# Performance work log

Measured on AMD Instinct MI355X. Metric: run time of the kernel, lower is better.

Reference implementation:

```python
import jax, jax.numpy as jnp
import numpy as np

HID = 128
HEADS = 8
HDIM = HID // HEADS
MLP = int(HID * 4.0)
N = 50000
E = 800000
EPS = 1e-6


def _ln(x):
    m = jnp.mean(x, axis=-1, keepdims=True)
    v = jnp.var(x, axis=-1, keepdims=True)
    return (x - m) / jnp.sqrt(v + EPS)


def _modulate(x, shift, scale):
    return x * (1 + scale) + shift


def setup_inputs() -> dict:
    key = jax.random.key(0)
    ks = jax.random.split(key, 12)
    s = lambda fan_in: 1.0 / np.sqrt(fan_in)
    return {
        "x": jax.random.normal(ks[0], (N, HID), dtype=jnp.float32),
        "edge_index": jax.random.randint(ks[1], (2, E), 0, N, dtype=jnp.int64),
        "c": jax.random.normal(ks[2], (N, HID), dtype=jnp.float32),
        "w_qkv": jax.random.normal(ks[3], (HID, 3 * HID), dtype=jnp.float32) * s(HID),
        "w_proj": jax.random.normal(ks[4], (HID, HID), dtype=jnp.float32) * s(HID),
        "b_proj": jnp.zeros((HID,), dtype=jnp.float32),
        "w_mlp1": jax.random.normal(ks[5], (HID, MLP), dtype=jnp.float32) * s(HID),
        "b_mlp1": jnp.zeros((MLP,), dtype=jnp.float32),
        "w_mlp2": jax.random.normal(ks[6], (MLP, HID), dtype=jnp.float32) * s(MLP),
        "b_mlp2": jnp.zeros((HID,), dtype=jnp.float32),
        "w_ada": jax.random.normal(ks[7], (HID, 6 * HID), dtype=jnp.float32) * s(HID),
        "b_ada": jnp.zeros((6 * HID,), dtype=jnp.float32),
    }


def _graph_attn(x, edge_index, w_qkv, w_proj, b_proj):
    n = x.shape[0]
    qkv = x @ w_qkv  # [N, 3*HID]
    q, k, v = jnp.split(qkv, 3, axis=-1)
    q = q.reshape(n, HEADS, HDIM)
    k = k.reshape(n, HEADS, HDIM)
    v = v.reshape(n, HEADS, HDIM)
    src = edge_index[0]  # j (source)
    dst = edge_index[1]  # i (destination / aggregation key)
    # per-edge attention score [E, HEADS]
    score = jnp.einsum('ehd,ehd->eh', q[dst], k[src]) / np.sqrt(HDIM)
    # segment softmax over destination node
    smax = jax.ops.segment_max(score, dst, num_segments=n)  # [N, H]
    ex = jnp.exp(score - smax[dst])
    den = jax.ops.segment_sum(ex, dst, num_segments=n)
    attn = ex / den[dst]  # [E, H]
    msg = v[src] * attn[:, :, None]  # [E, H, D]
    out = jax.ops.segment_sum(msg, dst, num_segments=n)  # [N, H, D]
    return out.reshape(n, HID) @ w_proj + b_proj


def reference(x, edge_index, c, w_qkv, w_proj, b_proj, w_mlp1, b_mlp1,
              w_mlp2, b_mlp2, w_ada, b_ada):
    mods = jax.nn.silu(c) @ w_ada + b_ada
    sh_msa, sc_msa, g_msa, sh_mlp, sc_mlp, g_mlp = jnp.split(mods, 6, axis=-1)
    x = x + g_msa * _graph_attn(_modulate(_ln(x), sh_msa, sc_msa),
                                edge_index, w_qkv, w_proj, b_proj)
    h = _modulate(_ln(x), sh_mlp, sc_mlp)
    h = jax.nn.gelu(h @ w_mlp1 + b_mlp1, approximate=True) @ w_mlp2 + b_mlp2
    return x + g_mlp * h
```

## Files before the change

kernel.cpp:

```cpp
#include <hip/hip_runtime.h>
#include <math.h>

#define N_NODES 50000
#define HIDD 128
#define HEADS 8
#define HDIM 16
#define NE 800000

using short8 = __attribute__((ext_vector_type(8))) short;
using f32x4 = __attribute__((ext_vector_type(4))) float;

__device__ __forceinline__ int load_idx(const void* ei, int is64, long long pos) {
  long long v = is64 ? ((const long long*)ei)[pos]
                     : (long long)((const int*)ei)[pos];
  unsigned uv = (unsigned)v;
  return (uv < N_NODES) ? (int)uv : 0;
}

__global__ void detect_kernel(const unsigned* __restrict__ ei_raw, int* flag) {
  __shared__ int any_nonzero;
  if (threadIdx.x == 0) any_nonzero = 0;
  __syncthreads();
  if (threadIdx.x < 128) {
    if (ei_raw[2 * threadIdx.x + 1] != 0u) atomicOr(&any_nonzero, 1);
  }
  __syncthreads();
  if (threadIdx.x == 0) *flag = any_nonzero ? 0 : 1;
}

__global__ __launch_bounds__(256) void probe_kernel(float* out, int n, float mb) {
  int i = blockIdx.x * 256 + threadIdx.x;
  if (i < n) out[i] = (i == 0) ? mb : 0.f;
}

struct ProNone {
  __device__ __forceinline__ float operator()(float v, int, int) const { return v; }
};
struct EpiNone {
  __device__ __forceinline__ float operator()(float a, int, int) const { return a; }
};
struct EpiBias {
  const float* b;
  __device__ __forceinline__ float operator()(float a, int, int c) const { return a + b[c]; }
};
struct EpiGelu {
  const float* b;
  __device__ __forceinline__ float operator()(float a, int, int c) const {
    float t = a + b[c];
    float u = 0.7978845608028654f * (t + 0.044715f * t * t * t);
    float au = fabsf(u);
    float e = __expf(2.f * au);
    float th = __builtin_copysignf(1.f - 2.f / (e + 1.f), u);
    return 0.5f * t * (1.f + th);
  }
};
struct EpiResGateB {
  const float* b;
  const float* xres;
  const unsigned short* gate;
  __device__ __forceinline__ float operator()(float a, int r, int c) const {
    float g = __uint_as_float((unsigned)gate[(size_t)r * 768 + c] << 16);
    return xres[(size_t)r * HIDD + c] + g * (a + b[c]);
  }
};

struct CvTab {
  int end[8];
  int src_sel[8];
  int src_off[8];
  int ldb[8];
  int n[8];
  int dst_off[8];
};
__global__ __launch_bounds__(256) void convert_all_kernel(
    const float* __restrict__ p0, const float* __restrict__ p1,
    const float* __restrict__ p2, const float* __restrict__ p3,
    const float* __restrict__ p4, CvTab t, int total,
    unsigned short* __restrict__ hi) {
  int idx = blockIdx.x * 256 + threadIdx.x;
  if (idx >= total) return;
  int s = 0;
#pragma unroll
  for (int j = 0; j < 7; j++) s += (idx >= t.end[j]) ? 1 : 0;
  int local = idx - (s ? t.end[s - 1] : 0);
  int N = t.n[s];
  int k = (unsigned)local / (unsigned)N;
  int n = local - k * N;
  const float* B;
  int sel = t.src_sel[s];
  B = (sel == 0) ? p0 : (sel == 1) ? p1 : (sel == 2) ? p2 : (sel == 3) ? p3 : p4;
  float f = B[(size_t)k * t.ldb[s] + t.src_off[s] + n];
  unsigned u = __float_as_uint(f);
  unsigned short hs = (unsigned short)((u + 0x7FFFu + ((u >> 16) & 1u)) >> 16);
  int lane = (((k >> 3) & 3) << 4) | (n & 15);
  int dst = t.dst_off[s] + (((k >> 5) * (N >> 4) + (n >> 4)) * 64 + lane) * 8 + (k & 7);
  hi[dst] = hs;
}

__device__ __forceinline__ void split8(const float f[8], short8& ahi, short8& alo) {
  union { unsigned u[4]; short8 v; } ch, cl;
#pragma unroll
  for (int e = 0; e < 4; e++) {
    unsigned u0 = __float_as_uint(f[2 * e]);
    unsigned u1 = __float_as_uint(f[2 * e + 1]);
    ch.u[e] = (u0 >> 16) | (u1 & 0xFFFF0000u);
    float h0 = __uint_as_float(u0 & 0xFFFF0000u);
    float h1 = __uint_as_float(u1 & 0xFFFF0000u);
    cl.u[e] = (__float_as_uint(f[2 * e] - h0) >> 16) |
              (__float_as_uint(f[2 * e + 1] - h1) & 0xFFFF0000u);
  }
  ahi = ch.v;
  alo = cl.v;
}

template <class Pro, int AMODE>
__device__ __forceinline__ void load_a_frag(
    const void* __restrict__ Av, const void* __restrict__ Av2, int arow, int K,
    int kb, int quad, bool aok, Pro pro, short8& ahi, short8& alo) {
  ahi = {};
  alo = {};
  if constexpr (AMODE == 0) {
    const float* A = (const float*)Av;
    float4 a0 = make_float4(0.f, 0.f, 0.f, 0.f), a1 = a0;
    if (aok) {
      const float* ap = A + (size_t)arow * K + kb * 32 + quad * 8;
      a0 = *(const float4*)ap;
      a1 = *(const float4*)(ap + 4);
      int cb = kb * 32 + quad * 8;
      a0.x = pro(a0.x, arow, cb + 0); a0.y = pro(a0.y, arow, cb + 1);
      a0.z = pro(a0.z, arow, cb + 2); a0.w = pro(a0.w, arow, cb + 3);
      a1.x = pro(a1.x, arow, cb + 4); a1.y = pro(a1.y, arow, cb + 5);
      a1.z = pro(a1.z, arow, cb + 6); a1.w = pro(a1.w, arow, cb + 7);
    }
    float f[8] = {a0.x, a0.y, a0.z, a0.w, a1.x, a1.y, a1.z, a1.w};
    split8(f, ahi, alo);
  } else if constexpr (AMODE == 1) {
    if (aok)
      ahi = *(const short8*)((const unsigned short*)Av + (size_t)arow * K + kb * 32 + quad * 8);
  } else {
    if (aok) {
      size_t aoff = (size_t)arow * K + kb * 32 + quad * 8;
      ahi = *(const short8*)((const unsigned short*)Av + aoff);
      alo = *(const short8*)((const unsigned short*)Av2 + aoff);
    }
  }
}

template <class Epi, int OMODE, int NTC>
__device__ __forceinline__ void store_tiles(
    const f32x4* acc, void* __restrict__ Cv, int M, int N, int mrow0, int col0,
    int quad, int ln15, Epi epi) {
  float* C = (float*)Cv;
#pragma unroll
  for (int nt = 0; nt < NTC; nt++) {
    f32x4 a = acc[nt];
    int gc = col0 + nt * 16 + ln15;
#pragma unroll
    for (int r = 0; r < 4; r++) {
      int gr = mrow0 + quad * 4 + r;
      if (gr < M) {
        if constexpr (OMODE == 1) {
          float* crow = C + (size_t)gr * 256;
          if (gc < 128) {
            crow[gc] = a[r];
          } else {
            unsigned u = __float_as_uint(a[r]);
            unsigned rr = (u + 0x7FFFu + ((u >> 16) & 1u)) >> 16;
            unsigned short* kv = (unsigned short*)crow + 256;
            int c = gc - 128;
            int idx = (c < 128) ? (((c >> 2) << 3) + (c & 3))
                                : ((((c - 128) >> 2) << 3) + 4 + ((c - 128) & 3));
            kv[idx] = (unsigned short)rr;
          }
        } else if constexpr (OMODE == 2) {
          float v = epi(a[r], gr, gc);
          unsigned u = __float_as_uint(v);
          unsigned rr = (u + 0x7FFFu + ((u >> 16) & 1u)) >> 16;
          ((unsigned short*)Cv)[(size_t)gr * N + gc] = (unsigned short)rr;
        } else {
          C[(size_t)gr * N + gc] = epi(a[r], gr, gc);
        }
      }
    }
  }
}

template <class Pro, class Epi, int OMODE, int AMODE, int NTC, int KK, bool LDSB = false>
__global__ __launch_bounds__(256) void gemm_direct(
    const void* __restrict__ Av, const void* __restrict__ Av2,
    const unsigned short* __restrict__ B,
    void* __restrict__ Cv, int M, int N, Pro pro, Epi epi) {
  const int tid = threadIdx.x;
  const int lane = tid & 63;
  const int wv = tid >> 6;
  const int quad = lane >> 4;
  const int ln15 = lane & 15;
  const int mrow0 = blockIdx.x * 64 + wv * 16;
  const int arow = mrow0 + ln15;
  const int Nt = N >> 4;
  const bool aok = (arow < M);
  const int col0 = blockIdx.y * (NTC * 16);
  const int ntbase = col0 >> 4;
  constexpr int KB = KK >> 5;
  static_assert(!LDSB || KB == 4, "LDSB path assumes K==128 (4 kb, one per wave)");

  __shared__ short8 lbs[LDSB ? 4 * NTC * 64 : 1];
  if constexpr (LDSB) {
    const unsigned short* gb = B + ((size_t)(wv * Nt + ntbase) * 64 + lane) * 8;
#pragma unroll
    for (int nt = 0; nt < NTC; nt++)
      lbs[(wv * NTC + nt) * 64 + lane] = *(const short8*)(gb + nt * 512);
    __syncthreads();
  }

  f32x4 acc[NTC] = {};
#pragma unroll
  for (int kb = 0; kb < KB; kb++) {
    short8 ahi, alo;
    load_a_frag<Pro, AMODE>(Av, Av2, arow, KK, kb, quad, aok, pro, ahi, alo);
    const unsigned short* bp = B + ((size_t)(kb * Nt + ntbase) * 64 + lane) * 8;
#pragma unroll
    for (int nt = 0; nt < NTC; nt++) {
      short8 b;
      if constexpr (LDSB)
        b = lbs[(kb * NTC + nt) * 64 + lane];
      else
        b = *(const short8*)(bp + nt * 512);
      if constexpr (AMODE != 1)
        acc[nt] = __builtin_amdgcn_mfma_f32_16x16x32_bf16(alo, b, acc[nt], 0, 0, 0);
      acc[nt] = __builtin_amdgcn_mfma_f32_16x16x32_bf16(ahi, b, acc[nt], 0, 0, 0);
    }
  }
  store_tiles<Epi, OMODE, NTC>(acc, Cv, M, N, mrow0, col0, quad, ln15, epi);
}

__global__ __launch_bounds__(256) void silu_split_kernel(
    const float* __restrict__ c, unsigned* __restrict__ ch, unsigned* __restrict__ cl) {
  int wave = threadIdx.x >> 6;
  int lane = threadIdx.x & 63;
  int row = blockIdx.x * 4 + wave;
  if (row >= N_NODES) return;
  float2 v = *(const float2*)(c + (size_t)row * HIDD + lane * 2);
  float ox = v.x / (1.f + __expf(-v.x));
  float oy = v.y / (1.f + __expf(-v.y));
  unsigned ux = __float_as_uint(ox), uy = __float_as_uint(oy);
  unsigned hx = ux & 0xFFFF0000u, hy = uy & 0xFFFF0000u;
  unsigned lx = __float_as_uint(ox - __uint_as_float(hx));
  unsigned ly = __float_as_uint(oy - __uint_as_float(hy));
  ch[(size_t)row * 64 + lane] = (ux >> 16) | hy;
  cl[(size_t)row * 64 + lane] = (lx >> 16) | (ly & 0xFFFF0000u);
}

__global__ __launch_bounds__(256) void ln_mod_kernel(
    const float* __restrict__ x, const unsigned* __restrict__ sa,
    unsigned* __restrict__ xh, unsigned* __restrict__ xl) {
  int wave = threadIdx.x >> 6;
  int lane = threadIdx.x & 63;
  int row = blockIdx.x * 4 + wave;
  if (row >= N_NODES) return;
  float2 v = *(const float2*)(x + (size_t)row * HIDD + lane * 2);
  float s = v.x + v.y;
  float sq = v.x * v.x + v.y * v.y;
#pragma unroll
  for (int o = 32; o >= 1; o >>= 1) {
    s += __shfl_xor(s, o);
    sq += __shfl_xor(sq, o);
  }
  float m = s * (1.f / 128.f);
  float var = sq * (1.f / 128.f) - m * m;
  float rs = rsqrtf(var + 1e-6f);
  unsigned shw = sa[(size_t)row * 384 + lane];
  unsigned scw = sa[(size_t)row * 384 + 64 + lane];
  float shx = __uint_as_float(shw << 16), shy = __uint_as_float(shw & 0xFFFF0000u);
  float scx = __uint_as_float(scw << 16), scy = __uint_as_float(scw & 0xFFFF0000u);
  float ox = (v.x - m) * rs * (1.f + scx) + shx;
  float oy = (v.y - m) * rs * (1.f + scy) + shy;
  unsigned ux = __float_as_uint(ox), uy = __float_as_uint(oy);
  unsigned hx = ux & 0xFFFF0000u, hy = uy & 0xFFFF0000u;
  unsigned lx = __float_as_uint(ox - __uint_as_float(hx));
  unsigned ly = __float_as_uint(oy - __uint_as_float(hy));
  xh[(size_t)row * 64 + lane] = (ux >> 16) | hy;
  xl[(size_t)row * 64 + lane] = (lx >> 16) | (ly & 0xFFFF0000u);
}

__global__ __launch_bounds__(256) void zero_int_kernel(int* p, int n) {
  int i = blockIdx.x * 256 + threadIdx.x;
  if (i < n) p[i] = 0;
}

__global__ __launch_bounds__(256) void hist_kernel(const void* __restrict__ ei,
                                                   const int* __restrict__ flag,
                                                   int* __restrict__ A) {
  int e = blockIdx.x * 256 + threadIdx.x;
  if (e >= NE) return;
  int dst = load_idx(ei, *flag, (long long)NE + e);
  atomicAdd(&A[dst + 1], 1);
}

__global__ __launch_bounds__(1024) void scan1_kernel(int* __restrict__ A, int n,
                                                     int* __restrict__ bsum) {
  __shared__ int buf[2][1024];
  int i = blockIdx.x * 1024 + threadIdx.x;
  int val = (i < n) ? A[i] : 0;
  int pb = 0;
  buf[0][threadIdx.x] = val;
  __syncthreads();
#pragma unroll
  for (int off = 1; off < 1024; off <<= 1) {
    int t = buf[pb][threadIdx.x];
    if ((int)threadIdx.x >= off) t += buf[pb][threadIdx.x - off];
    buf[pb ^ 1][threadIdx.x] = t;
    pb ^= 1;
    __syncthreads();
  }
  int incl = buf[pb][threadIdx.x];
  if (i < n) A[i] = incl;
  if (threadIdx.x == 1023) bsum[blockIdx.x] = incl;
}
__global__ void scan2_kernel(int* __restrict__ bsum, int nb) {
  int l = threadIdx.x;
  int v = (l < nb) ? bsum[l] : 0;
#pragma unroll
  for (int off = 1; off < 64; off <<= 1) {
    int t = __shfl_up(v, off);
    if (l >= off) v += t;
  }
  if (l < nb) bsum[l] = v;
}
__global__ __launch_bounds__(256) void scan3_kernel(int* __restrict__ A, int n,
                                                    const int* __restrict__ bsum) {
  int i = blockIdx.x * 256 + threadIdx.x;
  int b = i >> 10;
  if (i < n && b > 0) A[i] += bsum[b - 1];
}

__global__ __launch_bounds__(256) void scatter_kernel(const void* __restrict__ ei,
                                                      const int* __restrict__ flag,
                                                      int* __restrict__ A,
                                                      unsigned short* __restrict__ col) {
  int e = blockIdx.x * 256 + threadIdx.x;
  if (e >= NE) return;
  int is64 = *flag;
  int src = load_idx(ei, is64, e);
  int dst = load_idx(ei, is64, (long long)NE + e);
  int pos = atomicAdd(&A[dst], 1);
  col[pos] = (unsigned short)src;
}

__global__ __launch_bounds__(256) void node_attn_kernel(
    const int* __restrict__ A, const unsigned short* __restrict__ col,
    const float* __restrict__ qkv, float* __restrict__ attn) {
  int wave = threadIdx.x >> 6;
  int lane = threadIdx.x & 63;
  int half = lane >> 5;
  int l32 = lane & 31;
  int node = blockIdx.x * 4 + wave;
  if (node >= N_NODES) return;
  int start = (node == 0) ? 0 : A[node - 1];
  int end = A[node];
  int deg = end - start;

  float4 q = *(const float4*)(qkv + (size_t)node * 256 + l32 * 4);
  float l = 0.f;
  float4 acc = make_float4(0.f, 0.f, 0.f, 0.f);

  if (deg > 0) {
    int itc = (deg + 1) >> 1;
    int last = end - 1;
    const unsigned* qu = (const unsigned*)qkv;
    auto eidx = [&](int it) {
      int e = start + 2 * it + half;
      return (e <= last) ? e : last;
    };
    int i2 = col[eidx(2)];
    uint4 kv0 = *(const uint4*)(qu + (size_t)col[eidx(0)] * 256 + 128 + 4 * l32);
    uint4 kv1 = *(const uint4*)(qu + (size_t)col[eidx(1)] * 256 + 128 + 4 * l32);
    for (int it = 0; it < itc; it++) {
      uint4 kv2 = *(const uint4*)(qu + (size_t)i2 * 256 + 128 + 4 * l32);
      i2 = col[eidx(it + 3)];
      float kx = __uint_as_float(kv0.x << 16);
      float ky = __uint_as_float(kv0.x & 0xFFFF0000u);
      float kz = __uint_as_float(kv0.y << 16);
      float kw = __uint_as_float(kv0.y & 0xFFFF0000u);
      float s = q.x * kx + q.y * ky + q.z * kz + q.w * kw;
      s += __shfl_xor(s, 1);
      s += __shfl_xor(s, 2);
      s *= 0.25f;
      bool valid = (start + 2 * it + half) < end;
      float w = valid ? __expf(fminf(s, 60.f)) : 0.f;
      float vx = __uint_as_float(kv0.z << 16);
      float vy = __uint_as_float(kv0.z & 0xFFFF0000u);
      float vz = __uint_as_float(kv0.w << 16);
      float vw = __uint_as_float(kv0.w & 0xFFFF0000u);
      l += w;
      acc.x += w * vx;
      acc.y += w * vy;
      acc.z += w * vz;
      acc.w += w * vw;
      kv0 = kv1;
      kv1 = kv2;
    }
  }
  l += __shfl_xor(l, 32);
  acc.x += __shfl_xor(acc.x, 32);
  acc.y += __shfl_xor(acc.y, 32);
  acc.z += __shfl_xor(acc.z, 32);
  acc.w += __shfl_xor(acc.w, 32);
  float inv = (l > 0.f) ? 1.f / l : 0.f;
  if (half == 0) {
    float4 o = make_float4(acc.x * inv, acc.y * inv, acc.z * inv, acc.w * inv);
    *(float4*)(attn + (size_t)node * HIDD + l32 * 4) = o;
  }
}

extern "C" void kernel_launch(void* const* d_in, const int* in_sizes, int n_in,
                              void* d_out, int out_size, void* d_ws, size_t ws_size,
                              hipStream_t stream) {
  const float* x      = (const float*)d_in[0];
  const void*  ei     = d_in[1];
  const float* c      = (const float*)d_in[2];
  const float* w_qkv  = (const float*)d_in[3];
  const float* w_proj = (const float*)d_in[4];
  const float* b_proj = (const float*)d_in[5];
  const float* w_mlp1 = (const float*)d_in[6];
  const float* b_mlp1 = (const float*)d_in[7];
  const float* w_mlp2 = (const float*)d_in[8];
  const float* b_mlp2 = (const float*)d_in[9];
  const float* w_ada  = (const float*)d_in[10];
  const float* b_ada  = (const float*)d_in[11];
  float* out = (float*)d_out;

  const size_t NM = (size_t)N_NODES;
  unsigned short* ada = (unsigned short*)d_ws;
  float* buf1 = (float*)(ada + NM * 768);
  float* buf2 = buf1 + NM * 128;
  int*   Arow  = (int*)(buf2 + NM * 256);
  unsigned short* col = (unsigned short*)(Arow + 50048);
  int*   eflag = (int*)(col + NE);
  int*   bsum  = eflag + 8;
  unsigned short* Bpl = (unsigned short*)(bsum + 64);
  unsigned* xh = (unsigned*)buf1;
  unsigned* xl = xh + NM * 64;
  float* attnb = buf1;
  unsigned* sch = (unsigned*)buf2;
  unsigned* scl = sch + NM * 64;
  float* qkv   = buf2;
  unsigned short* h1 = (unsigned short*)buf2;

  const int o_qkv = 0, o_ada = 49152, o_proj = 147456, o_mlp1 = 163840,
            o_mlp2 = 229376;
  const int cv_total = 294912;

  const size_t req_bytes = (NM * 768) * 4 + 50048 * 4 + NE * 2 + 32 + 256 +
                           (size_t)cv_total * 2;
  dim3 blk(256);
  if (ws_size < req_bytes) {
    probe_kernel<<<dim3((out_size + 255) / 256), blk, 0, stream>>>(
        out, out_size, (float)(ws_size >> 20));
    return;
  }

  const int MB = (N_NODES + 63) / 64;
  const int EB = (NE + 255) / 256;
  const int SB = (N_NODES + 1 + 1023) / 1024;

  detect_kernel<<<dim3(1), blk, 0, stream>>>((const unsigned*)ei, eflag);
  zero_int_kernel<<<dim3((N_NODES + 1 + 255) / 256), blk, 0, stream>>>(Arow, N_NODES + 1);
  hist_kernel<<<dim3(EB), blk, 0, stream>>>(ei, eflag, Arow);
  scan1_kernel<<<dim3(SB), dim3(1024), 0, stream>>>(Arow, N_NODES + 1, bsum);
  scan2_kernel<<<dim3(1), dim3(64), 0, stream>>>(bsum, SB);
  scan3_kernel<<<dim3((N_NODES + 1 + 255) / 256), blk, 0, stream>>>(Arow, N_NODES + 1, bsum);
  scatter_kernel<<<dim3(EB), blk, 0, stream>>>(ei, eflag, Arow, col);

  {
    CvTab t;
    int sel[8]     = { 0,      1,      2,      3,      4,      0, 0, 0 };
    int soff[8]    = { 0,      0,      0,      0,      0,      0, 0, 0 };
    int ldb[8]     = { 384,    768,    128,    512,    128,    1, 1, 1 };
    int nn[8]      = { 384,    768,    128,    512,    128,    1, 1, 1 };
    int doff[8]    = { o_qkv,  o_ada,  o_proj, o_mlp1, o_mlp2, 0, 0, 0 };
    int cnt[8]     = { 49152,  98304,  16384,  65536,  65536,  0, 0, 0 };
    int accum = 0;
    for (int s = 0; s < 8; s++) {
      accum += cnt[s];
      t.end[s] = accum; t.src_sel[s] = sel[s]; t.src_off[s] = soff[s];
      t.ldb[s] = ldb[s]; t.n[s] = nn[s]; t.dst_off[s] = doff[s];
    }
    convert_all_kernel<<<dim3((cv_total + 255) / 256), blk, 0, stream>>>(
        w_qkv, w_ada, w_proj, w_mlp1, w_mlp2, t, cv_total, Bpl);
  }

  silu_split_kernel<<<dim3((N_NODES + 3) / 4), blk, 0, stream>>>(c, sch, scl);

  gemm_direct<ProNone, EpiBias, 2, 2, 8, 128, true><<<dim3(MB, 6), blk, 0, stream>>>(
      sch, scl, Bpl + o_ada, ada, N_NODES, 768, ProNone{}, EpiBias{b_ada});

  ln_mod_kernel<<<dim3((N_NODES + 3) / 4), blk, 0, stream>>>(
      x, (const unsigned*)ada, xh, xl);

  gemm_direct<ProNone, EpiNone, 1, 2, 8, 128, true><<<dim3(MB, 3), blk, 0, stream>>>(
      xh, xl, Bpl + o_qkv, qkv, N_NODES, 384, ProNone{}, EpiNone{});

  node_attn_kernel<<<dim3((N_NODES + 3) / 4), blk, 0, stream>>>(Arow, col, qkv, attnb);

  gemm_direct<ProNone, EpiResGateB, 0, 0, 4, 128, true><<<dim3(MB, 2), blk, 0, stream>>>(
      attnb, nullptr, Bpl + o_proj, out, N_NODES, 128,
      ProNone{}, EpiResGateB{b_proj, x, ada + 256});

  ln_mod_kernel<<<dim3((N_NODES + 3) / 4), blk, 0, stream>>>(
      out, (const unsigned*)(ada + 384), xh, xl);

  gemm_direct<ProNone, EpiGelu, 2, 2, 8, 128, true><<<dim3(MB, 4), blk, 0, stream>>>(
      xh, xl, Bpl + o_mlp1, h1, N_NODES, 512, ProNone{}, EpiGelu{b_mlp1});

  gemm_direct<ProNone, EpiResGateB, 0, 1, 4, 512, false><<<dim3(MB, 2), blk, 0, stream>>>(
      h1, nullptr, Bpl + o_mlp2, out, N_NODES, 128,
      ProNone{}, EpiResGateB{b_mlp2, out, ada + 640});
}
```

Measured before the change: 502.1 us.

## Process four edges per wave with 8-wide K/V interleave in node attention

Changes the bf16 K/V interleave written by the QKV GEMM epilogue from groups of 4 to groups of 8 elements. The node attention kernel now has each 16-lane quarter handle one edge, so a wave processes four edges per iteration instead of two. Each lane loads 8 K and 8 V values, which removes one shuffle from the score reduction. The aim is more edges in flight per wave and fewer loop iterations on the gather-bound aggregation, at the cost of more registers and more final cross-lane reductions.

```diff
diff --git a/kernel.cpp b/kernel.cpp
--- a/kernel.cpp
+++ b/kernel.cpp
@@ -9,6 +9,9 @@
 
 using short8 = __attribute__((ext_vector_type(8))) short;
 using f32x4 = __attribute__((ext_vector_type(4))) float;
+
+__device__ __forceinline__ float bf_lo(unsigned u) { return __uint_as_float(u << 16); }
+__device__ __forceinline__ float bf_hi(unsigned u) { return __uint_as_float(u & 0xFFFF0000u); }
 
 __device__ __forceinline__ int load_idx(const void* ei, int is64, long long pos) {
   long long v = is64 ? ((const long long*)ei)[pos]
@@ -168,8 +171,8 @@
             unsigned rr = (u + 0x7FFFu + ((u >> 16) & 1u)) >> 16;
             unsigned short* kv = (unsigned short*)crow + 256;
             int c = gc - 128;
-            int idx = (c < 128) ? (((c >> 2) << 3) + (c & 3))
-                                : ((((c - 128) >> 2) << 3) + 4 + ((c - 128) & 3));
+            int idx = (c < 128) ? (((c >> 3) << 4) + (c & 7))
+                                : ((((c - 128) >> 3) << 4) + 8 + ((c - 128) & 7));
             kv[idx] = (unsigned short)rr;
           }
         } else if constexpr (OMODE == 2) {
@@ -352,64 +355,73 @@
     const float* __restrict__ qkv, float* __restrict__ attn) {
   int wave = threadIdx.x >> 6;
   int lane = threadIdx.x & 63;
-  int half = lane >> 5;
-  int l32 = lane & 31;
+  int qtr = lane >> 4;
+  int l16 = lane & 15;
   int node = blockIdx.x * 4 + wave;
   if (node >= N_NODES) return;
   int start = (node == 0) ? 0 : A[node - 1];
   int end = A[node];
   int deg = end - start;
 
-  float4 q = *(const float4*)(qkv + (size_t)node * 256 + l32 * 4);
+  const float* qp = qkv + (size_t)node * 256 + l16 * 8;
+  float4 q0 = *(const float4*)qp;
+  float4 q1 = *(const float4*)(qp + 4);
   float l = 0.f;
-  float4 acc = make_float4(0.f, 0.f, 0.f, 0.f);
+  float4 a0 = make_float4(0.f, 0.f, 0.f, 0.f);
+  float4 a1 = make_float4(0.f, 0.f, 0.f, 0.f);
 
   if (deg > 0) {
-    int itc = (deg + 1) >> 1;
+    int itc = (deg + 3) >> 2;
     int last = end - 1;
     const unsigned* qu = (const unsigned*)qkv;
     auto eidx = [&](int it) {
-      int e = start + 2 * it + half;
+      int e = start + 4 * it + qtr;
       return (e <= last) ? e : last;
     };
     int i2 = col[eidx(2)];
-    uint4 kv0 = *(const uint4*)(qu + (size_t)col[eidx(0)] * 256 + 128 + 4 * l32);
-    uint4 kv1 = *(const uint4*)(qu + (size_t)col[eidx(1)] * 256 + 128 + 4 * l32);
+    const unsigned* b0 = qu + (size_t)col[eidx(0)] * 256 + 128 + 8 * l16;
+    uint4 k0 = *(const uint4*)b0;
+    uint4 v0 = *(const uint4*)(b0 + 4);
+    const unsigned* b1 = qu + (size_t)col[eidx(1)] * 256 + 128 + 8 * l16;
+    uint4 k1 = *(const uint4*)b1;
+    uint4 v1 = *(const uint4*)(b1 + 4);
     for (int it = 0; it < itc; it++) {
-      uint4 kv2 = *(const uint4*)(qu + (size_t)i2 * 256 + 128 + 4 * l32);
+      const unsigned* b2 = qu + (size_t)i2 * 256 + 128 + 8 * l16;
+      uint4 k2 = *(const uint4*)b2;
+      uint4 v2 = *(const uint4*)(b2 + 4);
       i2 = col[eidx(it + 3)];
-      float kx = __uint_as_float(kv0.x << 16);
-      float ky = __uint_as_float(kv0.x & 0xFFFF0000u);
-      float kz = __uint_as_float(kv0.y << 16);
-      float kw = __uint_as_float(kv0.y & 0xFFFF0000u);
-      float s = q.x * kx + q.y * ky + q.z * kz + q.w * kw;
+      float s = q0.x * bf_lo(k0.x) + q0.y * bf_hi(k0.x) +
+                q0.z * bf_lo(k0.y) + q0.w * bf_hi(k0.y) +
+                q1.x * bf_lo(k0.z) + q1.y * bf_hi(k0.z) +
+                q1.z * bf_lo(k0.w) + q1.w * bf_hi(k0.w);
       s += __shfl_xor(s, 1);
-      s += __shfl_xor(s, 2);
       s *= 0.25f;
-      bool valid = (start + 2 * it + half) < end;
+      bool valid = (start + 4 * it + qtr) < end;
       float w = valid ? __expf(fminf(s, 60.f)) : 0.f;
-      float vx = __uint_as_float(kv0.z << 16);
-      float vy = __uint_as_float(kv0.z & 0xFFFF0000u);
-      float vz = __uint_as_float(kv0.w << 16);
-      float vw = __uint_as_float(kv0.w & 0xFFFF0000u);
       l += w;
-      acc.x += w * vx;
-      acc.y += w * vy;
-      acc.z += w * vz;
-      acc.w += w * vw;
-      kv0 = kv1;
-      kv1 = kv2;
+      a0.x += w * bf_lo(v0.x); a0.y += w * bf_hi(v0.x);
+      a0.z += w * bf_lo(v0.y); a0.w += w * bf_hi(v0.y);
+      a1.x += w * bf_lo(v0.z); a1.y += w * bf_hi(v0.z);
+      a1.z += w * bf_lo(v0.w); a1.w += w * bf_hi(v0.w);
+      k0 = k1; v0 = v1;
+      k1 = k2; v1 = v2;
     }
   }
+  l += __shfl_xor(l, 16);
   l += __shfl_xor(l, 32);
-  acc.x += __shfl_xor(acc.x, 32);
-  acc.y += __shfl_xor(acc.y, 32);
-  acc.z += __shfl_xor(acc.z, 32);
-  acc.w += __shfl_xor(acc.w, 32);
+  a0.x += __shfl_xor(a0.x, 16); a0.x += __shfl_xor(a0.x, 32);
+  a0.y += __shfl_xor(a0.y, 16); a0.y += __shfl_xor(a0.y, 32);
+  a0.z += __shfl_xor(a0.z, 16); a0.z += __shfl_xor(a0.z, 32);
+  a0.w += __shfl_xor(a0.w, 16); a0.w += __shfl_xor(a0.w, 32);
+  a1.x += __shfl_xor(a1.x, 16); a1.x += __shfl_xor(a1.x, 32);
+  a1.y += __shfl_xor(a1.y, 16); a1.y += __shfl_xor(a1.y, 32);
+  a1.z += __shfl_xor(a1.z, 16); a1.z += __shfl_xor(a1.z, 32);
+  a1.w += __shfl_xor(a1.w, 16); a1.w += __shfl_xor(a1.w, 32);
   float inv = (l > 0.f) ? 1.f / l : 0.f;
-  if (half == 0) {
-    float4 o = make_float4(acc.x * inv, acc.y * inv, acc.z * inv, acc.w * inv);
-    *(float4*)(attn + (size_t)node * HIDD + l32 * 4) = o;
+  if (qtr == 0) {
+    float* op = attn + (size_t)node * HIDD + l16 * 8;
+    *(float4*)op = make_float4(a0.x * inv, a0.y * inv, a0.z * inv, a0.w * inv);
+    *(float4*)(op + 4) = make_float4(a1.x * inv, a1.y * inv, a1.z * inv, a1.w * inv);
   }
 }
 
```

After: 498.5 us. Within noise of the previous version (-0.7%).
